# Kernel tuning notes

Hardware: AMD Instinct MI355X
Metric: run time of the kernel (lower is better)

The kernel has to match this reference:

```python
import jax, jax.numpy as jnp
import numpy as np

N_NODES = 100000
N_EDGES = 1000000
N_GRAPHS = 16
D_NODE = 64
D_EDGE = 32
D_GLOB = 32
OUT_DIM = 64
IN1 = 2 * D_NODE + D_EDGE + D_GLOB  # 192
IN2 = D_NODE + OUT_DIM + D_GLOB     # 160


def setup_inputs() -> dict:
    key = jax.random.key(0)
    ks = jax.random.split(key, 9)
    x = jax.random.normal(ks[0], (N_NODES, D_NODE), dtype=jnp.float32)
    edge_index = jax.random.randint(ks[1], (2, N_EDGES), 0, N_NODES, dtype=jnp.int64 if jax.config.jax_enable_x64 else jnp.int32)
    edge_attr = jax.random.normal(ks[2], (N_EDGES, D_EDGE), dtype=jnp.float32)
    u = jax.random.normal(ks[3], (N_GRAPHS, D_GLOB), dtype=jnp.float32)
    batch = jnp.sort(jax.random.randint(ks[4], (N_NODES,), 0, N_GRAPHS))
    # Linear params (kaiming-ish scale)
    W1 = jax.random.normal(ks[5], (IN1, OUT_DIM), dtype=jnp.float32) / np.sqrt(IN1)
    b1 = jnp.zeros((OUT_DIM,), dtype=jnp.float32)
    W2 = jax.random.normal(ks[6], (IN2, OUT_DIM), dtype=jnp.float32) / np.sqrt(IN2)
    b2 = jnp.zeros((OUT_DIM,), dtype=jnp.float32)
    return {"x": x, "edge_index": edge_index, "edge_attr": edge_attr, "u": u,
            "batch": batch, "W1": W1, "b1": b1, "W2": W2, "b2": b2}


def reference(x, edge_index, edge_attr, u, batch, W1, b1, W2, b2):
    src = edge_index[0]  # [E]
    dst = edge_index[1]  # [E]
    u_per_node = u[batch]  # [N, Du] gather globals to nodes
    # gather-concat: [E, 2D + De + Du]
    all_feat = jnp.concatenate([x[dst], x[src], edge_attr, u_per_node[dst]], axis=-1)
    # mlp_1 + ReLU on every edge message
    msg = jax.nn.relu(all_feat @ W1 + b1)  # [E, out]
    # scatter-sum to destination nodes
    agg = jax.ops.segment_sum(msg, dst, num_segments=x.shape[0])  # [N, out]
    # mlp_2 + ReLU on nodes
    node_in = jnp.concatenate([x, agg, u_per_node], axis=-1)  # [N, D + out + Du]
    return jax.nn.relu(node_in @ W2 + b2)
```

## Files before the change

kernel.cpp:

```cpp
#include <hip/hip_runtime.h>

constexpr int N_NODES = 100000;
constexpr int N_EDGES = 1000000;
constexpr int D_NODE  = 64;
constexpr int D_EDGE  = 32;
constexpr int D_GLOB  = 32;
constexpr int OUT_DIM = 64;
constexpr int K1 = 2*D_NODE + D_EDGE + D_GLOB;
constexpr int K2 = D_NODE + OUT_DIM + D_GLOB;

typedef _Float16 f16x8 __attribute__((ext_vector_type(8)));
typedef unsigned short ushort8_t __attribute__((ext_vector_type(8)));
typedef float floatx16 __attribute__((ext_vector_type(16)));

constexpr int FS = 200;

constexpr size_t WS_W1T = 0;
constexpr size_t WS_W2T = 24576;
constexpr size_t WS_UB  = 45056;
constexpr size_t WS_XB  = 46080;

__device__ inline unsigned pack_f2(float a, float b) {
    auto h = __builtin_amdgcn_cvt_pkrtz(a, b);
    return __builtin_bit_cast(unsigned, h);
}

__global__ __launch_bounds__(256) void prep_kernel(
    const float* __restrict__ x, const float* __restrict__ u,
    const float* __restrict__ W1, const float* __restrict__ W2,
    unsigned short* __restrict__ ws_w1t, unsigned short* __restrict__ ws_w2t,
    unsigned short* __restrict__ ws_ub, unsigned short* __restrict__ ws_xb,
    float* __restrict__ out)
{
    const int t = blockIdx.x * 256 + threadIdx.x;
    const int stride = gridDim.x * 256;
    const float4* x4 = (const float4*)x;
    for (int i = t; i < N_NODES * 16; i += stride) {
        float4 v = x4[i];
        uint2 pk;
        pk.x = pack_f2(v.x, v.y);
        pk.y = pack_f2(v.z, v.w);
        *(uint2*)&ws_xb[i * 4] = pk;
    }
    const uint4 z = {0, 0, 0, 0};
    uint4* o4 = (uint4*)out;
    for (int i = t; i < N_NODES * 16; i += stride)
        o4[i] = z;
    for (int i = t; i < K1 * 64; i += stride) {
        int k = i >> 6, n = i & 63;
        _Float16 h = (_Float16)W1[i];
        ws_w1t[n * K1 + k] = __builtin_bit_cast(unsigned short, h);
    }
    for (int i = t; i < K2 * 64; i += stride) {
        int k = i >> 6, n = i & 63;
        _Float16 h = (_Float16)W2[i];
        ws_w2t[n * K2 + k] = __builtin_bit_cast(unsigned short, h);
    }
    for (int i = t; i < 16 * D_GLOB; i += stride) {
        _Float16 h = (_Float16)u[i];
        ws_ub[i] = __builtin_bit_cast(unsigned short, h);
    }
}

__global__ __launch_bounds__(256, 6) void edge_kernel(
    const unsigned short* __restrict__ xb, const int* __restrict__ ei,
    const float* __restrict__ ea, const unsigned short* __restrict__ ub,
    const int* __restrict__ batch, const unsigned short* __restrict__ W1t,
    const float* __restrict__ b1, float* __restrict__ out)
{
    __shared__ __align__(16) unsigned short smem[64 * FS];
    __shared__ int s_dst[64];
    __shared__ int s_src[64];
    __shared__ int s_b[64];

    const int tid  = threadIdx.x;
    const int lane = tid & 63;
    const int wv   = tid >> 6;
    const int tile = blockIdx.x;
    const int eh   = wv >> 1;
    const int nh   = wv & 1;
    const int col  = lane & 31;
    const int half = lane >> 5;
    const float4* ea4 = (const float4*)ea;

    if (tid < 64) {
        int e = tile * 64 + tid;
        int d = ei[N_EDGES + e];
        s_dst[tid] = d;
        s_src[tid] = ei[e];
        s_b[tid]   = batch[d];
    }

    {
        int el = tid >> 2, c = tid & 3;
        float4 v0 = ea4[(tile*64 + el) * 8 + c * 2 + 0];
        float4 v1 = ea4[(tile*64 + el) * 8 + c * 2 + 1];
        uint4 pk;
        pk.x = pack_f2(v0.x, v0.y); pk.y = pack_f2(v0.z, v0.w);
        pk.z = pack_f2(v1.x, v1.y); pk.w = pack_f2(v1.z, v1.w);
        *(uint4*)&smem[el * FS + (16 + c) * 8] = pk;
    }

    f16x8 Wf[12];
    #pragma unroll
    for (int s = 0; s < 12; ++s)
        Wf[s] = __builtin_bit_cast(f16x8,
            *(const ushort8_t*)&W1t[(nh*32 + col) * K1 + s*16 + half*8]);

    const int chp = (lane & 31) * 2;
    const float2 bv = *(const float2*)&b1[chp];

    __syncthreads();

    for (int q = tid; q < 64 * 20; q += 256) {
        int el = q / 20;
        int c  = q - el * 20;
        uint4 pk;
        if (c < 8)       pk = *(const uint4*)&xb[s_dst[el] * 64 + c * 8];
        else if (c < 16) pk = *(const uint4*)&xb[s_src[el] * 64 + (c - 8) * 8];
        else             pk = *(const uint4*)&ub[s_b[el] * 32 + (c - 16) * 8];
        *(uint4*)&smem[el * FS + (c < 16 ? c : c + 4) * 8] = pk;
    }
    __syncthreads();

    floatx16 acc = {0,0,0,0,0,0,0,0,0,0,0,0,0,0,0,0};
    #pragma unroll
    for (int s = 0; s < 12; ++s) {
        f16x8 a = __builtin_bit_cast(f16x8,
            *(const ushort8_t*)&smem[(eh*32 + col) * FS + s*16 + half*8]);
        acc = __builtin_amdgcn_mfma_f32_32x32x16_f16(a, Wf[s], acc, 0, 0, 0);
    }

    __syncthreads();
    float* smemf = (float*)smem;
    #pragma unroll
    for (int r = 0; r < 16; ++r) {
        int e = eh*32 + (r & 3) + 8*(r >> 2) + 4*half;
        smemf[e * 64 + nh*32 + col] = acc[r];
    }
    __syncthreads();

    #pragma unroll
    for (int it = 0; it < 8; ++it) {
        int e = wv*16 + it*2 + half;
        float2 m = *(const float2*)&smemf[e * 64 + chp];
        float v0 = m.x + bv.x; v0 = v0 > 0.f ? v0 : 0.f;
        float v1 = m.y + bv.y; v1 = v1 > 0.f ? v1 : 0.f;
        unsigned pk = pack_f2(v0, v1);
        unsigned short* p = (unsigned short*)out + (size_t)s_dst[e] * 128 + chp;
        asm volatile("global_atomic_pk_add_f16 %0, %1, off"
                     :: "v"(p), "v"(pk) : "memory");
    }
}

__global__ __launch_bounds__(256, 6) void node_kernel(
    const unsigned short* __restrict__ xb, const unsigned short* __restrict__ ub,
    const int* __restrict__ batch, const unsigned short* __restrict__ W2t,
    const float* __restrict__ b2, float* __restrict__ out)
{
    __shared__ __align__(16) unsigned short smem[64 * FS];
    __shared__ int s_b[64];

    const int tid  = threadIdx.x;
    const int lane = tid & 63;
    const int wv   = tid >> 6;
    const int base = blockIdx.x * 64;
    const int eh   = wv >> 1;
    const int nh   = wv & 1;
    const int col  = lane & 31;
    const int half = lane >> 5;

    if (tid < 64) {
        int n = base + tid;
        s_b[tid] = (n < N_NODES) ? batch[n] : 0;
    }

    f16x8 Bf[10];
    #pragma unroll
    for (int s = 0; s < 10; ++s)
        Bf[s] = __builtin_bit_cast(f16x8,
            *(const ushort8_t*)&W2t[(nh*32 + col) * K2 + s*16 + half*8]);
    const float b2v = b2[nh*32 + col];

    __syncthreads();

    const unsigned short* aggb = (const unsigned short*)out;
    for (int q = tid; q < 64 * 20; q += 256) {
        int nl = q / 20;
        int c  = q - nl * 20;
        int n  = base + nl;
        uint4 pk;
        if (n >= N_NODES) pk = uint4{0, 0, 0, 0};
        else if (c < 8)   pk = *(const uint4*)&xb[n * 64 + c * 8];
        else if (c < 16)  pk = *(const uint4*)&aggb[(size_t)n * 128 + (c - 8) * 8];
        else              pk = *(const uint4*)&ub[s_b[nl] * 32 + (c - 16) * 8];
        *(uint4*)&smem[nl * FS + c * 8] = pk;
    }
    __syncthreads();

    floatx16 acc = {0,0,0,0,0,0,0,0,0,0,0,0,0,0,0,0};
    #pragma unroll
    for (int s = 0; s < 10; ++s) {
        f16x8 a = __builtin_bit_cast(f16x8,
            *(const ushort8_t*)&smem[(eh*32 + col) * FS + s*16 + half*8]);
        acc = __builtin_amdgcn_mfma_f32_32x32x16_f16(a, Bf[s], acc, 0, 0, 0);
    }

    #pragma unroll
    for (int r = 0; r < 16; ++r) {
        int n = base + eh*32 + (r & 3) + 8*(r >> 2) + 4*half;
        if (n < N_NODES) {
            float vv = acc[r] + b2v;
            out[n * 64 + nh*32 + col] = vv > 0.f ? vv : 0.f;
        }
    }
}

extern "C" void kernel_launch(void* const* d_in, const int* in_sizes, int n_in,
                              void* d_out, int out_size, void* d_ws, size_t ws_size,
                              hipStream_t stream) {
    const float* x     = (const float*)d_in[0];
    const int*   ei    = (const int*)d_in[1];
    const float* ea    = (const float*)d_in[2];
    const float* u     = (const float*)d_in[3];
    const int*   batch = (const int*)d_in[4];
    const float* W1    = (const float*)d_in[5];
    const float* b1    = (const float*)d_in[6];
    const float* W2    = (const float*)d_in[7];
    const float* b2    = (const float*)d_in[8];
    float* out = (float*)d_out;

    unsigned short* ws_w1t = (unsigned short*)((char*)d_ws + WS_W1T);
    unsigned short* ws_w2t = (unsigned short*)((char*)d_ws + WS_W2T);
    unsigned short* ws_ub  = (unsigned short*)((char*)d_ws + WS_UB);
    unsigned short* ws_xb  = (unsigned short*)((char*)d_ws + WS_XB);

    prep_kernel<<<2048, 256, 0, stream>>>(x, u, W1, W2, ws_w1t, ws_w2t,
                                          ws_ub, ws_xb, out);
    edge_kernel<<<N_EDGES / 64, 256, 0, stream>>>(ws_xb, ei, ea, ws_ub, batch, ws_w1t, b1, out);
    node_kernel<<<(N_NODES + 63) / 64, 256, 0, stream>>>(ws_xb, ws_ub, batch, ws_w2t, b2, out);
}
```

Baseline: 360.1 us.

## Make edge kernel wave-independent with per-wave tiles and 16x16x32 MFMA

Restructures the edge kernel so each wave owns 16 edges end to end: it gathers their features into its own shared-memory segment, runs four 16x16x32 MFMAs per k-step over all 64 output columns, and scatters atomics. Block-wide __syncthreads are replaced by s_waitcnt lgkmcnt(0) fences, which removes cross-wave barrier stalls. In exchange, W1 fragments are reloaded from global memory for every edge tile instead of staying in registers. Relying on a wave-level waitcnt fence for cross-lane LDS visibility rests on lockstep wave execution.

```diff
diff --git a/kernel.cpp b/kernel.cpp
--- a/kernel.cpp
+++ b/kernel.cpp
@@ -12,6 +12,7 @@
 typedef _Float16 f16x8 __attribute__((ext_vector_type(8)));
 typedef unsigned short ushort8_t __attribute__((ext_vector_type(8)));
 typedef float floatx16 __attribute__((ext_vector_type(16)));
+typedef float f32x4 __attribute__((ext_vector_type(4)));
 
 constexpr int FS = 200;
 
@@ -23,6 +24,10 @@
 __device__ inline unsigned pack_f2(float a, float b) {
     auto h = __builtin_amdgcn_cvt_pkrtz(a, b);
     return __builtin_bit_cast(unsigned, h);
+}
+
+__device__ inline void wave_lds_fence() {
+    asm volatile("s_waitcnt lgkmcnt(0)" ::: "memory");
 }
 
 __global__ __launch_bounds__(256) void prep_kernel(
@@ -68,86 +73,81 @@
     const int* __restrict__ batch, const unsigned short* __restrict__ W1t,
     const float* __restrict__ b1, float* __restrict__ out)
 {
-    __shared__ __align__(16) unsigned short smem[64 * FS];
-    __shared__ int s_dst[64];
-    __shared__ int s_src[64];
-    __shared__ int s_b[64];
+    __shared__ __align__(16) unsigned short feat[4][16 * FS];
+    __shared__ int s_idx[4][3][16];
 
     const int tid  = threadIdx.x;
     const int lane = tid & 63;
     const int wv   = tid >> 6;
-    const int tile = blockIdx.x;
-    const int eh   = wv >> 1;
-    const int nh   = wv & 1;
-    const int col  = lane & 31;
-    const int half = lane >> 5;
+    const int t0   = blockIdx.x * 64 + wv * 16;
     const float4* ea4 = (const float4*)ea;
 
-    if (tid < 64) {
-        int e = tile * 64 + tid;
-        int d = ei[N_EDGES + e];
-        s_dst[tid] = d;
-        s_src[tid] = ei[e];
-        s_b[tid]   = batch[d];
-    }
+    unsigned short* fseg = feat[wv];
 
     {
-        int el = tid >> 2, c = tid & 3;
-        float4 v0 = ea4[(tile*64 + el) * 8 + c * 2 + 0];
-        float4 v1 = ea4[(tile*64 + el) * 8 + c * 2 + 1];
+        int el = lane >> 2, c = lane & 3;
+        float4 v0 = ea4[(size_t)(t0 + el) * 8 + c * 2 + 0];
+        float4 v1 = ea4[(size_t)(t0 + el) * 8 + c * 2 + 1];
         uint4 pk;
         pk.x = pack_f2(v0.x, v0.y); pk.y = pack_f2(v0.z, v0.w);
         pk.z = pack_f2(v1.x, v1.y); pk.w = pack_f2(v1.z, v1.w);
-        *(uint4*)&smem[el * FS + (16 + c) * 8] = pk;
-    }
-
-    f16x8 Wf[12];
-    #pragma unroll
-    for (int s = 0; s < 12; ++s)
-        Wf[s] = __builtin_bit_cast(f16x8,
-            *(const ushort8_t*)&W1t[(nh*32 + col) * K1 + s*16 + half*8]);
-
-    const int chp = (lane & 31) * 2;
-    const float2 bv = *(const float2*)&b1[chp];
-
-    __syncthreads();
-
-    for (int q = tid; q < 64 * 20; q += 256) {
+        *(uint4*)&fseg[el * FS + (16 + c) * 8] = pk;
+    }
+
+    if (lane < 16) {
+        int e = t0 + lane;
+        int d = ei[N_EDGES + e];
+        s_idx[wv][0][lane] = d;
+        s_idx[wv][1][lane] = ei[e];
+        s_idx[wv][2][lane] = batch[d];
+    }
+    wave_lds_fence();
+
+    for (int q = lane; q < 16 * 20; q += 64) {
         int el = q / 20;
         int c  = q - el * 20;
         uint4 pk;
-        if (c < 8)       pk = *(const uint4*)&xb[s_dst[el] * 64 + c * 8];
-        else if (c < 16) pk = *(const uint4*)&xb[s_src[el] * 64 + (c - 8) * 8];
-        else             pk = *(const uint4*)&ub[s_b[el] * 32 + (c - 16) * 8];
-        *(uint4*)&smem[el * FS + (c < 16 ? c : c + 4) * 8] = pk;
-    }
-    __syncthreads();
-
-    floatx16 acc = {0,0,0,0,0,0,0,0,0,0,0,0,0,0,0,0};
-    #pragma unroll
-    for (int s = 0; s < 12; ++s) {
+        if (c < 8)       pk = *(const uint4*)&xb[(size_t)s_idx[wv][0][el] * 64 + c * 8];
+        else if (c < 16) pk = *(const uint4*)&xb[(size_t)s_idx[wv][1][el] * 64 + (c - 8) * 8];
+        else             pk = *(const uint4*)&ub[s_idx[wv][2][el] * 32 + (c - 16) * 8];
+        *(uint4*)&fseg[el * FS + (c < 16 ? c : c + 4) * 8] = pk;
+    }
+    wave_lds_fence();
+
+    const int arow = lane & 15;
+    const int kb   = lane >> 4;
+    f32x4 acc[4] = {{0,0,0,0}, {0,0,0,0}, {0,0,0,0}, {0,0,0,0}};
+    #pragma unroll
+    for (int ks = 0; ks < 6; ++ks) {
         f16x8 a = __builtin_bit_cast(f16x8,
-            *(const ushort8_t*)&smem[(eh*32 + col) * FS + s*16 + half*8]);
-        acc = __builtin_amdgcn_mfma_f32_32x32x16_f16(a, Wf[s], acc, 0, 0, 0);
-    }
-
-    __syncthreads();
-    float* smemf = (float*)smem;
-    #pragma unroll
-    for (int r = 0; r < 16; ++r) {
-        int e = eh*32 + (r & 3) + 8*(r >> 2) + 4*half;
-        smemf[e * 64 + nh*32 + col] = acc[r];
-    }
-    __syncthreads();
-
+            *(const ushort8_t*)&fseg[arow * FS + ks * 32 + kb * 8]);
+        #pragma unroll
+        for (int g = 0; g < 4; ++g) {
+            f16x8 b = __builtin_bit_cast(f16x8,
+                *(const ushort8_t*)&W1t[(g * 16 + arow) * K1 + ks * 32 + kb * 8]);
+            acc[g] = __builtin_amdgcn_mfma_f32_16x16x32_f16(a, b, acc[g], 0, 0, 0);
+        }
+    }
+    wave_lds_fence();
+
+    float* mseg = (float*)fseg;
+    #pragma unroll
+    for (int g = 0; g < 4; ++g)
+        #pragma unroll
+        for (int r = 0; r < 4; ++r)
+            mseg[((lane >> 4) * 4 + r) * 64 + g * 16 + (lane & 15)] = acc[g][r];
+    wave_lds_fence();
+
+    const int chp = (lane & 31) * 2;
+    const float2 bv = *(const float2*)&b1[chp];
     #pragma unroll
     for (int it = 0; it < 8; ++it) {
-        int e = wv*16 + it*2 + half;
-        float2 m = *(const float2*)&smemf[e * 64 + chp];
+        int el = it * 2 + (lane >> 5);
+        float2 m = *(const float2*)&mseg[el * 64 + chp];
         float v0 = m.x + bv.x; v0 = v0 > 0.f ? v0 : 0.f;
         float v1 = m.y + bv.y; v1 = v1 > 0.f ? v1 : 0.f;
         unsigned pk = pack_f2(v0, v1);
-        unsigned short* p = (unsigned short*)out + (size_t)s_dst[e] * 128 + chp;
+        unsigned short* p = (unsigned short*)out + (size_t)s_idx[wv][0][el] * 128 + chp;
         asm volatile("global_atomic_pk_add_f16 %0, %1, off"
                      :: "v"(p), "v"(pk) : "memory");
     }
```

Result: slower. 414.9 us (+15.2%).

## Load edge GEMM operands directly from global into MFMA registers, bypass LDS staging

Applied to the files above, without the earlier changes.

The edge kernel no longer stages gathered node, edge and global features in shared memory. Each lane now loads its MFMA A-fragments straight from global memory using its own edge's indices, and loads W1 fragments per k-step instead of preloading all twelve. This removes one barrier and the LDS round-trip, and shrinks shared memory, which may allow more resident blocks. The prep kernel now zeroes only the half of the output rows that the f16 atomic accumulator uses. The cost is less coalesced global gathers, since each lane reads a 16-byte piece of a different row, and W1 is re-read from cache on every k-step.

```diff
diff --git a/kernel.cpp b/kernel.cpp
--- a/kernel.cpp
+++ b/kernel.cpp
@@ -44,8 +44,10 @@
     }
     const uint4 z = {0, 0, 0, 0};
     uint4* o4 = (uint4*)out;
-    for (int i = t; i < N_NODES * 16; i += stride)
-        o4[i] = z;
+    for (int i = t; i < N_NODES * 8; i += stride) {
+        int n = i >> 3, c = i & 7;
+        o4[n * 16 + c] = z;
+    }
     for (int i = t; i < K1 * 64; i += stride) {
         int k = i >> 6, n = i & 63;
         _Float16 h = (_Float16)W1[i];
@@ -68,7 +70,7 @@
     const int* __restrict__ batch, const unsigned short* __restrict__ W1t,
     const float* __restrict__ b1, float* __restrict__ out)
 {
-    __shared__ __align__(16) unsigned short smem[64 * FS];
+    __shared__ __align__(16) float msg[64 * 64];
     __shared__ int s_dst[64];
     __shared__ int s_src[64];
     __shared__ int s_b[64];
@@ -81,7 +83,6 @@
     const int nh   = wv & 1;
     const int col  = lane & 31;
     const int half = lane >> 5;
-    const float4* ea4 = (const float4*)ea;
 
     if (tid < 64) {
         int e = tile * 64 + tid;
@@ -91,59 +92,61 @@
         s_b[tid]   = batch[d];
     }
 
-    {
-        int el = tid >> 2, c = tid & 3;
-        float4 v0 = ea4[(tile*64 + el) * 8 + c * 2 + 0];
-        float4 v1 = ea4[(tile*64 + el) * 8 + c * 2 + 1];
+    const int er = eh * 32 + col;
+
+    f16x8 a_ea[2];
+    #pragma unroll
+    for (int s = 0; s < 2; ++s) {
+        const float* ep = &ea[((size_t)(tile * 64) + er) * 32 + s * 16 + half * 8];
+        float4 v0 = *(const float4*)ep;
+        float4 v1 = *(const float4*)(ep + 4);
         uint4 pk;
         pk.x = pack_f2(v0.x, v0.y); pk.y = pack_f2(v0.z, v0.w);
         pk.z = pack_f2(v1.x, v1.y); pk.w = pack_f2(v1.z, v1.w);
-        *(uint4*)&smem[el * FS + (16 + c) * 8] = pk;
-    }
-
-    f16x8 Wf[12];
-    #pragma unroll
-    for (int s = 0; s < 12; ++s)
-        Wf[s] = __builtin_bit_cast(f16x8,
-            *(const ushort8_t*)&W1t[(nh*32 + col) * K1 + s*16 + half*8]);
+        a_ea[s] = __builtin_bit_cast(f16x8, pk);
+    }
 
     const int chp = (lane & 31) * 2;
     const float2 bv = *(const float2*)&b1[chp];
 
     __syncthreads();
 
-    for (int q = tid; q < 64 * 20; q += 256) {
-        int el = q / 20;
-        int c  = q - el * 20;
-        uint4 pk;
-        if (c < 8)       pk = *(const uint4*)&xb[s_dst[el] * 64 + c * 8];
-        else if (c < 16) pk = *(const uint4*)&xb[s_src[el] * 64 + (c - 8) * 8];
-        else             pk = *(const uint4*)&ub[s_b[el] * 32 + (c - 16) * 8];
-        *(uint4*)&smem[el * FS + (c < 16 ? c : c + 4) * 8] = pk;
-    }
-    __syncthreads();
+    const int d  = s_dst[er];
+    const int sc = s_src[er];
+    const int bb = s_b[er];
+    const unsigned short* wrow = &W1t[(nh * 32 + col) * K1];
 
     floatx16 acc = {0,0,0,0,0,0,0,0,0,0,0,0,0,0,0,0};
     #pragma unroll
     for (int s = 0; s < 12; ++s) {
-        f16x8 a = __builtin_bit_cast(f16x8,
-            *(const ushort8_t*)&smem[(eh*32 + col) * FS + s*16 + half*8]);
-        acc = __builtin_amdgcn_mfma_f32_32x32x16_f16(a, Wf[s], acc, 0, 0, 0);
-    }
-
-    __syncthreads();
-    float* smemf = (float*)smem;
+        f16x8 a;
+        if (s < 4)
+            a = __builtin_bit_cast(f16x8,
+                *(const ushort8_t*)&xb[(size_t)d * 64 + s * 16 + half * 8]);
+        else if (s < 8)
+            a = __builtin_bit_cast(f16x8,
+                *(const ushort8_t*)&xb[(size_t)sc * 64 + (s - 4) * 16 + half * 8]);
+        else if (s < 10)
+            a = a_ea[s - 8];
+        else
+            a = __builtin_bit_cast(f16x8,
+                *(const ushort8_t*)&ub[bb * 32 + (s - 10) * 16 + half * 8]);
+        f16x8 b = __builtin_bit_cast(f16x8,
+            *(const ushort8_t*)&wrow[s * 16 + half * 8]);
+        acc = __builtin_amdgcn_mfma_f32_32x32x16_f16(a, b, acc, 0, 0, 0);
+    }
+
     #pragma unroll
     for (int r = 0; r < 16; ++r) {
         int e = eh*32 + (r & 3) + 8*(r >> 2) + 4*half;
-        smemf[e * 64 + nh*32 + col] = acc[r];
+        msg[e * 64 + nh*32 + col] = acc[r];
     }
     __syncthreads();
 
     #pragma unroll
     for (int it = 0; it < 8; ++it) {
         int e = wv*16 + it*2 + half;
-        float2 m = *(const float2*)&smemf[e * 64 + chp];
+        float2 m = *(const float2*)&msg[e * 64 + chp];
         float v0 = m.x + bv.x; v0 = v0 > 0.f ? v0 : 0.f;
         float v1 = m.y + bv.y; v1 = v1 > 0.f ? v1 : 0.f;
         unsigned pk = pack_f2(v0, v1);
```

After: 428.5 us. 19.0% more time.
